# Kernel optimization log

Measured on AMD Instinct MI355X. Metric: run time of the kernel, lower is better.

Reference implementation:

```python
import jax, jax.numpy as jnp
import numpy as np

B = 4096
D = 256
N = 9000000
ALPHA = 0.5      # alpha_weight
GAMMA_S = 0.8
GAMMA_U = 0.9
RHO = 6.0
EPS = 1e-14
ETA = 0.01
TAU_MIN = 0.001
TAU_MAX = 1.0
GRAD_CLIP = 5.0
TAU_INIT = 0.07


def setup_inputs() -> dict:
    key = jax.random.key(0)
    k1, k2 = jax.random.split(key)
    return {
        "zis": jax.random.normal(k1, (B, D), dtype=jnp.float32),
        "zjs": jax.random.normal(k2, (B, D), dtype=jnp.float32),
        "ids": jnp.arange(B, dtype=jnp.int32),
        "s_I": jnp.zeros(N, jnp.float32),
        "s_T": jnp.zeros(N, jnp.float32),
        "b_I": jnp.zeros(N, jnp.float32),
        "b_T": jnp.zeros(N, jnp.float32),
        "u_I": jnp.zeros(N, jnp.float32),
        "u_T": jnp.zeros(N, jnp.float32),
        "tau_I": jnp.full(N, TAU_INIT, jnp.float32),
        "tau_T": jnp.full(N, TAU_INIT, jnp.float32),
    }


def reference(zis, zjs, ids, s_I, s_T, b_I, b_T, u_I, u_T, tau_I, tau_T):
    sg = jax.lax.stop_gradient
    Bc = zis.shape[0]
    # normalize
    zis = zis / jnp.linalg.norm(zis, axis=1, keepdims=True)
    zjs = zjs / jnp.linalg.norm(zjs, axis=1, keepdims=True)
    sim = jnp.einsum('id,jd->ij', zis, zjs)                 # [B,B]
    diag = jnp.diagonal(sim)
    image_diffs = sim - diag[:, None]
    text_diffs = sim - diag[None, :]
    tau_i = tau_I[ids]
    tau_t = tau_T[ids]
    # detached temperature-scaled diffs (torch .detach())
    idt = sg(image_diffs) / tau_i[:, None]
    tdt = sg(text_diffs) / tau_t[None, :]
    # running max update (online log-sum-exp shift)
    old_b_i = b_I[ids]
    old_b_t = b_T[ids]
    new_b_i = jnp.maximum(old_b_i, idt.max(axis=1))
    new_b_t = jnp.maximum(old_b_t, tdt.max(axis=0))
    mask = 1.0 - jnp.eye(Bc, dtype=zis.dtype)
    exp_i = jnp.exp(idt - new_b_i[:, None]) * mask
    exp_t = jnp.exp(tdt - new_b_t[None, :]) * mask
    g_i = exp_i.sum(axis=1)                                  # [B]
    g_t = exp_t.sum(axis=0)                                  # [B]
    # EMA of normalizers, rescaled by max shift
    s_i = (1.0 - GAMMA_S) * s_I[ids] * jnp.exp(old_b_i - new_b_i) + GAMMA_S * g_i
    s_t = (1.0 - GAMMA_S) * s_T[ids] * jnp.exp(old_b_t - new_b_t) + GAMMA_S * g_t
    s_i_c = jnp.clip(s_i, EPS, None)[:, None]                # [B,1]
    s_t_c = jnp.clip(s_t, EPS, None)[None, :]                # [1,B]
    w_i = exp_i / s_i_c
    w_t = exp_t / s_t_c
    image_loss = (sg(w_i) * image_diffs).sum(axis=1)         # [B]
    text_loss = (sg(w_t) * text_diffs).sum(axis=0)           # [B]
    total_loss = ALPHA * image_loss.mean() + (1.0 - ALPHA) * text_loss.mean()
    grad_tau_image = jnp.log(s_i_c) + new_b_i[:, None] + RHO - (w_i * idt).sum(axis=1, keepdims=True) / (Bc - 1)
    grad_tau_text = jnp.log(s_t_c) + new_b_t[None, :] + RHO - (w_t * tdt).sum(axis=0, keepdims=True) / (Bc - 1)
    # EMA of tau gradients with clipping, then temperature update
    u_i = (1.0 - GAMMA_U) * u_I[ids] + GAMMA_U * jnp.clip(grad_tau_image[:, 0], -GRAD_CLIP, GRAD_CLIP)
    u_t = (1.0 - GAMMA_U) * u_T[ids] + GAMMA_U * jnp.clip(grad_tau_text[0, :], -GRAD_CLIP, GRAD_CLIP)
    tau_i_new = jnp.clip(tau_i - ETA * u_i, TAU_MIN, TAU_MAX)
    tau_t_new = jnp.clip(tau_t - ETA * u_t, TAU_MIN, TAU_MAX)
    # scatter updated state back into persistent buffers
    s_I = s_I.at[ids].set(s_i)
    s_T = s_T.at[ids].set(s_t)
    b_I = b_I.at[ids].set(new_b_i)
    b_T = b_T.at[ids].set(new_b_t)
    u_I = u_I.at[ids].set(u_i)
    u_T = u_T.at[ids].set(u_t)
    tau_I = tau_I.at[ids].set(tau_i_new)
    tau_T = tau_T.at[ids].set(tau_t_new)
    return (g_i[:, None], g_t[None, :], grad_tau_image, grad_tau_text, total_loss,
            tau_i.mean(), tau_t.mean(), s_I, s_T, b_I, b_T, u_I, u_T, tau_I, tau_T)
```

## Files before the change

kernel.cpp:

```cpp
#include <hip/hip_runtime.h>
#include <math.h>

#define BDIM 4096
#define DDIM 256
#define NSTATE 9000000
#define PREFIX 3674116
#define PREFIX_N4 918529
#define COPY_THREADS 1048576

#define C_ALPHA 0.5f
#define C_GAMMA_S 0.8f
#define C_GAMMA_U 0.9f
#define C_RHO 6.0f
#define C_EPS 1e-14f
#define C_ETA 0.01f
#define C_TAU_MIN 0.001f
#define C_TAU_MAX 1.0f
#define C_GRAD_CLIP 5.0f

typedef unsigned short u16;
typedef __attribute__((ext_vector_type(8))) short short8;
typedef __attribute__((ext_vector_type(16))) float f32x16;
typedef __attribute__((ext_vector_type(4))) float nf4;

#define MFMA32 __builtin_amdgcn_mfma_f32_32x32x16_bf16

__device__ inline u16 f2bf(float f) {
    unsigned u = __float_as_uint(f);
    unsigned r = (u + 0x7FFFu + ((u >> 16) & 1u)) >> 16;
    return (u16)r;
}
__device__ inline float bf2f(u16 h) { return __uint_as_float(((unsigned)h) << 16); }

__device__ inline void nt_copy4(const nf4* __restrict__ s, long k, float* __restrict__ dbase) {
    nf4 v = __builtin_nontemporal_load(&s[k]);
    float* dp = dbase + 4 * k;
    __builtin_nontemporal_store(v.x, dp + 0);
    __builtin_nontemporal_store(v.y, dp + 1);
    __builtin_nontemporal_store(v.z, dp + 2);
    __builtin_nontemporal_store(v.w, dp + 3);
}

__global__ __launch_bounds__(256) void kprep(const float* __restrict__ zis,
                                             const float* __restrict__ zjs,
                                             u16* __restrict__ Ah, u16* __restrict__ Al,
                                             u16* __restrict__ Bh, u16* __restrict__ Bl,
                                             const int* __restrict__ ids,
                                             const float* __restrict__ tau_I,
                                             const float* __restrict__ tau_T,
                                             float* __restrict__ rowIT,
                                             float* __restrict__ colIT,
                                             float* __restrict__ acc4,
                                             int* __restrict__ ticket) {
    int blk = blockIdx.x;
    int t = threadIdx.x;
    if (blk == 256) {
        float sI = 0.f, sT = 0.f;
        for (int i = t; i < BDIM; i += 256) {
            int id = ids[i];
            float ti = tau_I[id], tt = tau_T[id];
            rowIT[i] = 1.0f / ti;
            colIT[i] = 1.0f / tt;
            sI += ti; sT += tt;
        }
        __shared__ float red[512];
        red[t] = sI; red[256 + t] = sT;
        __syncthreads();
        for (int s = 128; s > 0; s >>= 1) {
            if (t < s) { red[t] += red[t + s]; red[256 + t] += red[256 + t + s]; }
            __syncthreads();
        }
        if (t == 0) {
            acc4[0] = 0.f;
            acc4[1] = 0.f;
            acc4[2] = red[0];
            acc4[3] = red[256];
            *ticket = 0;
        }
        return;
    }
    bool isB = blk >= 128;
    const float* Z = isB ? zjs : zis;
    u16* H = isB ? Bh : Ah;
    u16* L = isB ? Bl : Al;
    int rblk = blk & 127;
    int r = t & 31, kc0 = t >> 5;
    int row = rblk * 32 + r;

    __shared__ float ssq[32];
    if (t < 32) ssq[t] = 0.f;
    __syncthreads();

    float4 v[8];
    float partial = 0.f;
#pragma unroll
    for (int c = 0; c < 4; ++c) {
        int kc = kc0 + 8 * c;
        float4 a = *(const float4*)&Z[(size_t)row * DDIM + kc * 8];
        float4 b = *(const float4*)&Z[(size_t)row * DDIM + kc * 8 + 4];
        v[2 * c] = a; v[2 * c + 1] = b;
        partial += a.x * a.x + a.y * a.y + a.z * a.z + a.w * a.w;
        partial += b.x * b.x + b.y * b.y + b.z * b.z + b.w * b.w;
    }
    atomicAdd(&ssq[r], partial);
    __syncthreads();
    float inv = rsqrtf(ssq[r]);

#pragma unroll
    for (int c = 0; c < 4; ++c) {
        int kc = kc0 + 8 * c;
        float f[8];
        f[0] = v[2*c].x * inv;   f[1] = v[2*c].y * inv;
        f[2] = v[2*c].z * inv;   f[3] = v[2*c].w * inv;
        f[4] = v[2*c+1].x * inv; f[5] = v[2*c+1].y * inv;
        f[6] = v[2*c+1].z * inv; f[7] = v[2*c+1].w * inv;
        u16 hh[8], ll[8];
#pragma unroll
        for (int j = 0; j < 8; ++j) {
            hh[j] = f2bf(f[j]);
            ll[j] = f2bf(f[j] - bf2f(hh[j]));
        }
        size_t base = (size_t)rblk * 8192 + (size_t)kc * 256 + (size_t)r * 8;
        uint4 ph, pl;
        ph.x = (unsigned)hh[0] | ((unsigned)hh[1] << 16);
        ph.y = (unsigned)hh[2] | ((unsigned)hh[3] << 16);
        ph.z = (unsigned)hh[4] | ((unsigned)hh[5] << 16);
        ph.w = (unsigned)hh[6] | ((unsigned)hh[7] << 16);
        pl.x = (unsigned)ll[0] | ((unsigned)ll[1] << 16);
        pl.y = (unsigned)ll[2] | ((unsigned)ll[3] << 16);
        pl.z = (unsigned)ll[4] | ((unsigned)ll[5] << 16);
        pl.w = (unsigned)ll[6] | ((unsigned)ll[7] << 16);
        *(uint4*)(H + base) = ph;
        *(uint4*)(L + base) = pl;
    }
}

__global__ __launch_bounds__(256, 3) void kmain(
    const u16* __restrict__ Ah, const u16* __restrict__ Al,
    const u16* __restrict__ Bh, const u16* __restrict__ Bl,
    const float* __restrict__ rowIT, const float* __restrict__ colIT,
    float* __restrict__ rPM, float* __restrict__ rPS1, float* __restrict__ rPS2,
    float* __restrict__ cPM, float* __restrict__ cPS1, float* __restrict__ cPS2,
    float* __restrict__ diag,
    const float* __restrict__ s_I, const float* __restrict__ s_T,
    const float* __restrict__ b_I, const float* __restrict__ b_T,
    const float* __restrict__ u_I, const float* __restrict__ u_T,
    const float* __restrict__ tau_I, const float* __restrict__ tau_T,
    long b0s, float* o)
{
    __shared__ float T[2][64 * 68];
    int bid = blockIdx.x;
    int t = threadIdx.x;

    if (bid % 5 != 0) {
        long cid = (long)(bid / 5) * 4 + (bid % 5) - 1;
        long tid = cid * 256 + t;
        {
            const nf4* s = (const nf4*)(s_I + b0s);
            float* d = o + b0s;
            long n4 = (NSTATE - b0s) / 4;
            for (long k = tid; k < n4; k += COPY_THREADS) nt_copy4(s, k, d);
        }
        const float* srcs[7] = {s_T, b_I, b_T, u_I, u_T, tau_I, tau_T};
#pragma unroll
        for (int b = 0; b < 7; b++) {
            const nf4* s = (const nf4*)srcs[b];
            float* d = o + (long)(b + 1) * NSTATE;
            for (long k = tid; k < NSTATE / 4; k += COPY_THREADS) nt_copy4(s, k, d);
        }
        return;
    }

    int gid = bid / 5;
    int by = gid >> 5, bx = gid & 31;
    int w = t >> 6, l = t & 63;
    int rw = w & 1, cw = w >> 1;
    int h = l >> 5, lc = l & 31;
    int rowbase = by * 128 + rw * 64;
    int colbase = bx * 128 + cw * 64;

    const u16* pAh = Ah + (size_t)(by * 4 + rw * 2) * 8192;
    const u16* pAl = Al + (size_t)(by * 4 + rw * 2) * 8192;
    const u16* pBh = Bh + (size_t)(bx * 4 + cw * 2) * 8192;
    const u16* pBl = Bl + (size_t)(bx * 4 + cw * 2) * 8192;

    f32x16 acc00, acc01, acc10, acc11;
#pragma unroll
    for (int e = 0; e < 16; ++e) { acc00[e] = 0.f; acc01[e] = 0.f; acc10[e] = 0.f; acc11[e] = 0.f; }

    for (int s = 0; s < 16; ++s) {
        int off = s * 512 + l * 8;
        short8 a0h = *(const short8*)(pAh + off);
        short8 a1h = *(const short8*)(pAh + 8192 + off);
        short8 a0l = *(const short8*)(pAl + off);
        short8 a1l = *(const short8*)(pAl + 8192 + off);
        short8 b0h = *(const short8*)(pBh + off);
        short8 b1h = *(const short8*)(pBh + 8192 + off);
        short8 b0l = *(const short8*)(pBl + off);
        short8 b1l = *(const short8*)(pBl + 8192 + off);

        acc00 = MFMA32(a0h, b0h, acc00, 0, 0, 0);
        acc01 = MFMA32(a0h, b1h, acc01, 0, 0, 0);
        acc10 = MFMA32(a1h, b0h, acc10, 0, 0, 0);
        acc11 = MFMA32(a1h, b1h, acc11, 0, 0, 0);
        acc00 = MFMA32(a0h, b0l, acc00, 0, 0, 0);
        acc01 = MFMA32(a0h, b1l, acc01, 0, 0, 0);
        acc10 = MFMA32(a1h, b0l, acc10, 0, 0, 0);
        acc11 = MFMA32(a1h, b1l, acc11, 0, 0, 0);
        acc00 = MFMA32(a0l, b0h, acc00, 0, 0, 0);
        acc01 = MFMA32(a0l, b1h, acc01, 0, 0, 0);
        acc10 = MFMA32(a1l, b0h, acc10, 0, 0, 0);
        acc11 = MFMA32(a1l, b1h, acc11, 0, 0, 0);
    }

#define COLPART(A0, A1, CT) do {                                                   \
        int gc = colbase + (CT) * 32 + lc;                                         \
        float itc = colIT[gc];                                                     \
        float m = -INFINITY;                                                       \
        _Pragma("unroll") for (int e = 0; e < 16; ++e) {                           \
            m = fmaxf(m, (A0)[e]); m = fmaxf(m, (A1)[e]); }                        \
        m = fmaxf(m, __shfl_xor(m, 32));                                           \
        float S1 = 0.f, S2 = 0.f;                                                  \
        _Pragma("unroll") for (int e = 0; e < 16; ++e) {                           \
            float v0 = (A0)[e]; float e0 = __expf((v0 - m) * itc); S1 += e0; S2 += e0 * v0; \
            float v1 = (A1)[e]; float e1 = __expf((v1 - m) * itc); S1 += e1; S2 += e1 * v1; } \
        S1 += __shfl_xor(S1, 32); S2 += __shfl_xor(S2, 32);                        \
        if (h == 0) { int slot = by * 2 + rw;                                      \
            cPM [slot * 4096 + gc] = m;                                            \
            cPS1[slot * 4096 + gc] = S1;                                           \
            cPS2[slot * 4096 + gc] = S2; }                                         \
    } while (0)

    COLPART(acc00, acc10, 0);
    COLPART(acc01, acc11, 1);

#define ROWPART(TB) do {                                                           \
        float* Tb = (TB);                                                          \
        _Pragma("unroll") for (int q = 0; q < 4; ++q) {                            \
            _Pragma("unroll") for (int j = 0; j < 4; ++j) {                        \
                int rr = 8 * q + 4 * h + j;                                        \
                Tb[(rr     ) * 68 + lc     ] = acc00[4 * q + j];                   \
                Tb[(rr     ) * 68 + lc + 32] = acc01[4 * q + j];                   \
                Tb[(rr + 32) * 68 + lc     ] = acc10[4 * q + j];                   \
                Tb[(rr + 32) * 68 + lc + 32] = acc11[4 * q + j]; } }               \
        float itr = rowIT[rowbase + l];                                            \
        float4 vv[16];                                                             \
        _Pragma("unroll") for (int c = 0; c < 16; ++c)                             \
            vv[c] = *(const float4*)&Tb[l * 68 + 4 * c];                           \
        float m = -INFINITY;                                                       \
        _Pragma("unroll") for (int c = 0; c < 16; ++c)                             \
            m = fmaxf(m, fmaxf(fmaxf(vv[c].x, vv[c].y), fmaxf(vv[c].z, vv[c].w))); \
        float S1 = 0.f, S2 = 0.f;                                                  \
        _Pragma("unroll") for (int c = 0; c < 16; ++c) {                           \
            float e0 = __expf((vv[c].x - m) * itr); S1 += e0; S2 += e0 * vv[c].x;  \
            float e1 = __expf((vv[c].y - m) * itr); S1 += e1; S2 += e1 * vv[c].y;  \
            float e2 = __expf((vv[c].z - m) * itr); S1 += e2; S2 += e2 * vv[c].z;  \
            float e3 = __expf((vv[c].w - m) * itr); S1 += e3; S2 += e3 * vv[c].w; }\
        int slot = bx * 2 + cw;                                                    \
        rPM [slot * 4096 + rowbase + l] = m;                                       \
        rPS1[slot * 4096 + rowbase + l] = S1;                                      \
        rPS2[slot * 4096 + rowbase + l] = S2;                                      \
        if (bx == by && rw == cw) diag[rowbase + l] = Tb[l * 68 + l];              \
    } while (0)

    if (w < 2) ROWPART(T[w]);
    __syncthreads();
    if (w >= 2) ROWPART(T[w - 2]);
}

__global__ __launch_bounds__(256) void kmerge(
    const int* __restrict__ ids,
    const float* __restrict__ s_I, const float* __restrict__ b_I,
    const float* __restrict__ u_I, const float* __restrict__ tau_I,
    const float* __restrict__ s_T, const float* __restrict__ b_T,
    const float* __restrict__ u_T, const float* __restrict__ tau_T,
    const float* __restrict__ rowIT, const float* __restrict__ colIT,
    const float* __restrict__ diag,
    const float* __restrict__ rPM, const float* __restrict__ rPS1, const float* __restrict__ rPS2,
    const float* __restrict__ cPM, const float* __restrict__ cPS1, const float* __restrict__ cPS2,
    float* __restrict__ O,
    float* __restrict__ sc_arrs,
    float* o_scat,
    float* acc4, int* ticket)
{
    int j = blockIdx.x * 256 + threadIdx.x;
    int t = threadIdx.x;
    bool rowside = (j < BDIM);
    int i = rowside ? j : j - BDIM;
    const float* PM  = rowside ? rPM  : cPM;
    const float* PS1 = rowside ? rPS1 : cPS1;
    const float* PS2 = rowside ? rPS2 : cPS2;
    float it = rowside ? rowIT[i] : colIT[i];

    float M = -INFINITY, S1 = 0.f, S2 = 0.f;
    for (int k = 0; k < 64; k++) {
        float m  = PM [k * BDIM + i];
        float s1 = PS1[k * BDIM + i];
        float s2 = PS2[k * BDIM + i];
        float Mn = fmaxf(M, m);
        float ea = __expf((M - Mn) * it);
        float eb = __expf((m - Mn) * it);
        S1 = S1 * ea + s1 * eb;
        S2 = S2 * ea + s2 * eb;
        M = Mn;
    }

    int id = ids[i];
    float tau  = rowside ? tau_I[id] : tau_T[id];
    float oldb = rowside ? b_I[id]   : b_T[id];
    float olds = rowside ? s_I[id]   : s_T[id];
    float oldu = rowside ? u_I[id]   : u_T[id];
    float dg = diag[i];

    float nb = fmaxf(oldb, (M - dg) * it);
    float F  = __expf((M - dg) * it - nb);
    float ed = __expf(-nb);
    float g  = F * S1 - ed;
    float Cs = F * (S2 - dg * S1);

    float s_new = (1.f - C_GAMMA_S) * olds * __expf(oldb - nb) + C_GAMMA_S * g;
    float scl = fmaxf(s_new, C_EPS);
    float loss = Cs / scl;
    float grad = logf(scl) + nb + C_RHO - (Cs / (scl * tau)) * (1.0f / (float)(BDIM - 1));
    float gc = fminf(fmaxf(grad, -C_GRAD_CLIP), C_GRAD_CLIP);
    float u_new = (1.f - C_GAMMA_U) * oldu + C_GAMMA_U * gc;
    float tau_new = fminf(fmaxf(tau - C_ETA * u_new, C_TAU_MIN), C_TAU_MAX);

    int bank0 = rowside ? 0 : 1;
    if (rowside) {
        O[i] = g;
        O[8192 + i] = grad;
    } else {
        O[4096 + i] = g;
        O[12288 + i] = grad;
    }
    if (o_scat) {
        long lid = id;
        o_scat[(long)(bank0 + 0) * NSTATE + lid] = s_new;
        o_scat[(long)(bank0 + 2) * NSTATE + lid] = nb;
        o_scat[(long)(bank0 + 4) * NSTATE + lid] = u_new;
        o_scat[(long)(bank0 + 6) * NSTATE + lid] = tau_new;
    } else {
        int base = rowside ? 0 : 4;
        sc_arrs[(base + 0) * BDIM + i] = s_new;
        sc_arrs[(base + 1) * BDIM + i] = nb;
        sc_arrs[(base + 2) * BDIM + i] = u_new;
        sc_arrs[(base + 3) * BDIM + i] = tau_new;
    }

    __shared__ float red[256];
    red[t] = loss;
    __syncthreads();
    for (int s = 128; s > 0; s >>= 1) {
        if (t < s) red[t] += red[t + s];
        __syncthreads();
    }
    if (t == 0) {
        atomicAdd(&acc4[rowside ? 0 : 1], red[0]);
        __threadfence();
        int old = atomicAdd(ticket, 1);
        if (old == 31) {
            float li = atomicAdd(&acc4[0], 0.f);
            float lt = atomicAdd(&acc4[1], 0.f);
            float invB = 1.0f / (float)BDIM;
            O[16384] = C_ALPHA * (li * invB) + (1.f - C_ALPHA) * (lt * invB);
            O[16385] = acc4[2] * invB;
            O[16386] = acc4[3] * invB;
        }
    }
}

__global__ __launch_bounds__(256) void kfix(const float* s_I, float* o) {
    long tid = (long)blockIdx.x * 256 + threadIdx.x;
    const nf4* s = (const nf4*)s_I;
    for (long k = tid; k < PREFIX_N4; k += 3584L * 256) nt_copy4(s, k, o);
}

__global__ __launch_bounds__(256) void kscat(const int* __restrict__ ids,
                                             const float* __restrict__ sc_arrs,
                                             float* __restrict__ o) {
    int t = blockIdx.x * 256 + threadIdx.x;
    if (t >= BDIM) return;
    long id = ids[t];
    o[0L * NSTATE + id] = sc_arrs[0 * BDIM + t];
    o[1L * NSTATE + id] = sc_arrs[4 * BDIM + t];
    o[2L * NSTATE + id] = sc_arrs[1 * BDIM + t];
    o[3L * NSTATE + id] = sc_arrs[5 * BDIM + t];
    o[4L * NSTATE + id] = sc_arrs[2 * BDIM + t];
    o[5L * NSTATE + id] = sc_arrs[6 * BDIM + t];
    o[6L * NSTATE + id] = sc_arrs[3 * BDIM + t];
    o[7L * NSTATE + id] = sc_arrs[7 * BDIM + t];
}

extern "C" void kernel_launch(void* const* d_in, const int* in_sizes, int n_in,
                              void* d_out, int out_size, void* d_ws, size_t ws_size,
                              hipStream_t stream) {
    const float* zis   = (const float*)d_in[0];
    const float* zjs   = (const float*)d_in[1];
    const int*   ids   = (const int*)d_in[2];
    const float* s_I   = (const float*)d_in[3];
    const float* s_T   = (const float*)d_in[4];
    const float* b_I   = (const float*)d_in[5];
    const float* b_T   = (const float*)d_in[6];
    const float* u_I   = (const float*)d_in[7];
    const float* u_T   = (const float*)d_in[8];
    const float* tau_I = (const float*)d_in[9];
    const float* tau_T = (const float*)d_in[10];
    float* O  = (float*)d_out;
    float* ws = (float*)d_ws;

    float* rowIT  = ws;
    float* colIT  = ws + 4096;
    float* acc4   = ws + 8192;
    int*   ticket = (int*)(ws + 8196);
    float* sc_arrs = ws + 16384;

    const bool bigws = ws_size >= (size_t)16 * 1024 * 1024;

    float *rPM, *rPS1, *rPS2, *cPM, *cPS1, *cPS2, *diag;
    u16 *Ah, *Al, *Bh, *Bl;
    long b0s;
    if (bigws) {
        float* P = ws + 53248;
        rPM  = P;            rPS1 = P + 262144;  rPS2 = P + 524288;
        cPM  = P + 786432;   cPS1 = P + 1048576; cPS2 = P + 1310720;
        diag = P + 1572864;
        Ah = (u16*)(P + 1576960);
        Al = Ah + 1048576; Bh = Al + 1048576; Bl = Bh + 1048576;
        b0s = 0;
    } else {
        float* P = O + 16388;
        rPM  = P;            rPS1 = P + 262144;  rPS2 = P + 524288;
        cPM  = P + 786432;   cPS1 = P + 1048576; cPS2 = P + 1310720;
        diag = P + 1572864;
        Ah = (u16*)(P + 1576960);
        Al = Ah + 1048576; Bh = Al + 1048576; Bl = Bh + 1048576;
        b0s = PREFIX;
    }

    kprep<<<257, 256, 0, stream>>>(zis, zjs, Ah, Al, Bh, Bl,
                                   ids, tau_I, tau_T, rowIT, colIT, acc4, ticket);

    kmain<<<5120, 256, 0, stream>>>(Ah, Al, Bh, Bl, rowIT, colIT,
                                    rPM, rPS1, rPS2, cPM, cPS1, cPS2, diag,
                                    s_I, s_T, b_I, b_T, u_I, u_T, tau_I, tau_T,
                                    b0s, O + 16387);

    kmerge<<<32, 256, 0, stream>>>(ids, s_I, b_I, u_I, tau_I, s_T, b_T, u_T, tau_T,
                                   rowIT, colIT, diag,
                                   rPM, rPS1, rPS2, cPM, cPS1, cPS2,
                                   O, sc_arrs, bigws ? (O + 16387) : nullptr,
                                   acc4, ticket);

    if (!bigws) {
        kfix<<<3584, 256, 0, stream>>>(s_I, O + 16387);
        kscat<<<16, 256, 0, stream>>>(ids, sc_arrs, O + 16387);
    }
}
```

Baseline: 544.4 us.

## Fuse all stages into one persistent kernel with atomic work queues

Replaces the prep, main GEMM/copy, merge, prefix-fix and scatter kernels with a single persistent kernel of 768 blocks. Blocks pull work items from atomic counters: normalization and bf16 split, GEMM tiles, 16K-float state-copy chunks, merge, prefix copy, then scatter, with spin-wait dependencies between phases. The aim is to remove launch gaps and let the bandwidth-bound copy overlap the MFMA tile work dynamically. It adds spin-wait synchronization costs and relies on all 768 blocks being co-resident to avoid deadlock.

```diff
diff --git a/kernel.cpp b/kernel.cpp
--- a/kernel.cpp
+++ b/kernel.cpp
@@ -3,10 +3,15 @@
 
 #define BDIM 4096
 #define DDIM 256
-#define NSTATE 9000000
-#define PREFIX 3674116
-#define PREFIX_N4 918529
-#define COPY_THREADS 1048576
+#define NSTATE 9000000L
+#define PREFIX 3674116L
+
+#define NTILES 1024
+#define CHUNK_F 16384L
+#define CPB 550
+#define NCHUNKS (8*CPB)
+#define NPFX 225
+#define GRID 768
 
 #define C_ALPHA 0.5f
 #define C_GAMMA_S 0.8f
@@ -24,6 +29,7 @@
 typedef __attribute__((ext_vector_type(4))) float nf4;
 
 #define MFMA32 __builtin_amdgcn_mfma_f32_32x32x16_bf16
+#define AGS __HIP_MEMORY_SCOPE_AGENT
 
 __device__ inline u16 f2bf(float f) {
     unsigned u = __float_as_uint(f);
@@ -40,178 +46,6 @@
     __builtin_nontemporal_store(v.z, dp + 2);
     __builtin_nontemporal_store(v.w, dp + 3);
 }
-
-__global__ __launch_bounds__(256) void kprep(const float* __restrict__ zis,
-                                             const float* __restrict__ zjs,
-                                             u16* __restrict__ Ah, u16* __restrict__ Al,
-                                             u16* __restrict__ Bh, u16* __restrict__ Bl,
-                                             const int* __restrict__ ids,
-                                             const float* __restrict__ tau_I,
-                                             const float* __restrict__ tau_T,
-                                             float* __restrict__ rowIT,
-                                             float* __restrict__ colIT,
-                                             float* __restrict__ acc4,
-                                             int* __restrict__ ticket) {
-    int blk = blockIdx.x;
-    int t = threadIdx.x;
-    if (blk == 256) {
-        float sI = 0.f, sT = 0.f;
-        for (int i = t; i < BDIM; i += 256) {
-            int id = ids[i];
-            float ti = tau_I[id], tt = tau_T[id];
-            rowIT[i] = 1.0f / ti;
-            colIT[i] = 1.0f / tt;
-            sI += ti; sT += tt;
-        }
-        __shared__ float red[512];
-        red[t] = sI; red[256 + t] = sT;
-        __syncthreads();
-        for (int s = 128; s > 0; s >>= 1) {
-            if (t < s) { red[t] += red[t + s]; red[256 + t] += red[256 + t + s]; }
-            __syncthreads();
-        }
-        if (t == 0) {
-            acc4[0] = 0.f;
-            acc4[1] = 0.f;
-            acc4[2] = red[0];
-            acc4[3] = red[256];
-            *ticket = 0;
-        }
-        return;
-    }
-    bool isB = blk >= 128;
-    const float* Z = isB ? zjs : zis;
-    u16* H = isB ? Bh : Ah;
-    u16* L = isB ? Bl : Al;
-    int rblk = blk & 127;
-    int r = t & 31, kc0 = t >> 5;
-    int row = rblk * 32 + r;
-
-    __shared__ float ssq[32];
-    if (t < 32) ssq[t] = 0.f;
-    __syncthreads();
-
-    float4 v[8];
-    float partial = 0.f;
-#pragma unroll
-    for (int c = 0; c < 4; ++c) {
-        int kc = kc0 + 8 * c;
-        float4 a = *(const float4*)&Z[(size_t)row * DDIM + kc * 8];
-        float4 b = *(const float4*)&Z[(size_t)row * DDIM + kc * 8 + 4];
-        v[2 * c] = a; v[2 * c + 1] = b;
-        partial += a.x * a.x + a.y * a.y + a.z * a.z + a.w * a.w;
-        partial += b.x * b.x + b.y * b.y + b.z * b.z + b.w * b.w;
-    }
-    atomicAdd(&ssq[r], partial);
-    __syncthreads();
-    float inv = rsqrtf(ssq[r]);
-
-#pragma unroll
-    for (int c = 0; c < 4; ++c) {
-        int kc = kc0 + 8 * c;
-        float f[8];
-        f[0] = v[2*c].x * inv;   f[1] = v[2*c].y * inv;
-        f[2] = v[2*c].z * inv;   f[3] = v[2*c].w * inv;
-        f[4] = v[2*c+1].x * inv; f[5] = v[2*c+1].y * inv;
-        f[6] = v[2*c+1].z * inv; f[7] = v[2*c+1].w * inv;
-        u16 hh[8], ll[8];
-#pragma unroll
-        for (int j = 0; j < 8; ++j) {
-            hh[j] = f2bf(f[j]);
-            ll[j] = f2bf(f[j] - bf2f(hh[j]));
-        }
-        size_t base = (size_t)rblk * 8192 + (size_t)kc * 256 + (size_t)r * 8;
-        uint4 ph, pl;
-        ph.x = (unsigned)hh[0] | ((unsigned)hh[1] << 16);
-        ph.y = (unsigned)hh[2] | ((unsigned)hh[3] << 16);
-        ph.z = (unsigned)hh[4] | ((unsigned)hh[5] << 16);
-        ph.w = (unsigned)hh[6] | ((unsigned)hh[7] << 16);
-        pl.x = (unsigned)ll[0] | ((unsigned)ll[1] << 16);
-        pl.y = (unsigned)ll[2] | ((unsigned)ll[3] << 16);
-        pl.z = (unsigned)ll[4] | ((unsigned)ll[5] << 16);
-        pl.w = (unsigned)ll[6] | ((unsigned)ll[7] << 16);
-        *(uint4*)(H + base) = ph;
-        *(uint4*)(L + base) = pl;
-    }
-}
-
-__global__ __launch_bounds__(256, 3) void kmain(
-    const u16* __restrict__ Ah, const u16* __restrict__ Al,
-    const u16* __restrict__ Bh, const u16* __restrict__ Bl,
-    const float* __restrict__ rowIT, const float* __restrict__ colIT,
-    float* __restrict__ rPM, float* __restrict__ rPS1, float* __restrict__ rPS2,
-    float* __restrict__ cPM, float* __restrict__ cPS1, float* __restrict__ cPS2,
-    float* __restrict__ diag,
-    const float* __restrict__ s_I, const float* __restrict__ s_T,
-    const float* __restrict__ b_I, const float* __restrict__ b_T,
-    const float* __restrict__ u_I, const float* __restrict__ u_T,
-    const float* __restrict__ tau_I, const float* __restrict__ tau_T,
-    long b0s, float* o)
-{
-    __shared__ float T[2][64 * 68];
-    int bid = blockIdx.x;
-    int t = threadIdx.x;
-
-    if (bid % 5 != 0) {
-        long cid = (long)(bid / 5) * 4 + (bid % 5) - 1;
-        long tid = cid * 256 + t;
-        {
-            const nf4* s = (const nf4*)(s_I + b0s);
-            float* d = o + b0s;
-            long n4 = (NSTATE - b0s) / 4;
-            for (long k = tid; k < n4; k += COPY_THREADS) nt_copy4(s, k, d);
-        }
-        const float* srcs[7] = {s_T, b_I, b_T, u_I, u_T, tau_I, tau_T};
-#pragma unroll
-        for (int b = 0; b < 7; b++) {
-            const nf4* s = (const nf4*)srcs[b];
-            float* d = o + (long)(b + 1) * NSTATE;
-            for (long k = tid; k < NSTATE / 4; k += COPY_THREADS) nt_copy4(s, k, d);
-        }
-        return;
-    }
-
-    int gid = bid / 5;
-    int by = gid >> 5, bx = gid & 31;
-    int w = t >> 6, l = t & 63;
-    int rw = w & 1, cw = w >> 1;
-    int h = l >> 5, lc = l & 31;
-    int rowbase = by * 128 + rw * 64;
-    int colbase = bx * 128 + cw * 64;
-
-    const u16* pAh = Ah + (size_t)(by * 4 + rw * 2) * 8192;
-    const u16* pAl = Al + (size_t)(by * 4 + rw * 2) * 8192;
-    const u16* pBh = Bh + (size_t)(bx * 4 + cw * 2) * 8192;
-    const u16* pBl = Bl + (size_t)(bx * 4 + cw * 2) * 8192;
-
-    f32x16 acc00, acc01, acc10, acc11;
-#pragma unroll
-    for (int e = 0; e < 16; ++e) { acc00[e] = 0.f; acc01[e] = 0.f; acc10[e] = 0.f; acc11[e] = 0.f; }
-
-    for (int s = 0; s < 16; ++s) {
-        int off = s * 512 + l * 8;
-        short8 a0h = *(const short8*)(pAh + off);
-        short8 a1h = *(const short8*)(pAh + 8192 + off);
-        short8 a0l = *(const short8*)(pAl + off);
-        short8 a1l = *(const short8*)(pAl + 8192 + off);
-        short8 b0h = *(const short8*)(pBh + off);
-        short8 b1h = *(const short8*)(pBh + 8192 + off);
-        short8 b0l = *(const short8*)(pBl + off);
-        short8 b1l = *(const short8*)(pBl + 8192 + off);
-
-        acc00 = MFMA32(a0h, b0h, acc00, 0, 0, 0);
-        acc01 = MFMA32(a0h, b1h, acc01, 0, 0, 0);
-        acc10 = MFMA32(a1h, b0h, acc10, 0, 0, 0);
-        acc11 = MFMA32(a1h, b1h, acc11, 0, 0, 0);
-        acc00 = MFMA32(a0h, b0l, acc00, 0, 0, 0);
-        acc01 = MFMA32(a0h, b1l, acc01, 0, 0, 0);
-        acc10 = MFMA32(a1h, b0l, acc10, 0, 0, 0);
-        acc11 = MFMA32(a1h, b1l, acc11, 0, 0, 0);
-        acc00 = MFMA32(a0l, b0h, acc00, 0, 0, 0);
-        acc01 = MFMA32(a0l, b1h, acc01, 0, 0, 0);
-        acc10 = MFMA32(a1l, b0h, acc10, 0, 0, 0);
-        acc11 = MFMA32(a1l, b1h, acc11, 0, 0, 0);
-    }
 
 #define COLPART(A0, A1, CT) do {                                                   \
         int gc = colbase + (CT) * 32 + lc;                                         \
@@ -230,9 +64,6 @@
             cPS1[slot * 4096 + gc] = S1;                                           \
             cPS2[slot * 4096 + gc] = S2; }                                         \
     } while (0)
-
-    COLPART(acc00, acc10, 0);
-    COLPART(acc01, acc11, 1);
 
 #define ROWPART(TB) do {                                                           \
         float* Tb = (TB);                                                          \
@@ -263,133 +94,370 @@
         if (bx == by && rw == cw) diag[rowbase + l] = Tb[l * 68 + l];              \
     } while (0)
 
-    if (w < 2) ROWPART(T[w]);
-    __syncthreads();
-    if (w >= 2) ROWPART(T[w - 2]);
+__global__ void kinit(float* ws) {
+    int t = threadIdx.x;
+    if (t < 12) ((int*)(ws + 8196))[t] = 0;
+    if (t == 12) ws[8192] = 0.f;
+    if (t == 13) ws[8193] = 0.f;
 }
 
-__global__ __launch_bounds__(256) void kmerge(
+__global__ __launch_bounds__(256, 3) void kall(
+    const float* __restrict__ zis, const float* __restrict__ zjs,
     const int* __restrict__ ids,
-    const float* __restrict__ s_I, const float* __restrict__ b_I,
-    const float* __restrict__ u_I, const float* __restrict__ tau_I,
-    const float* __restrict__ s_T, const float* __restrict__ b_T,
-    const float* __restrict__ u_T, const float* __restrict__ tau_T,
-    const float* __restrict__ rowIT, const float* __restrict__ colIT,
-    const float* __restrict__ diag,
-    const float* __restrict__ rPM, const float* __restrict__ rPS1, const float* __restrict__ rPS2,
-    const float* __restrict__ cPM, const float* __restrict__ cPS1, const float* __restrict__ cPS2,
-    float* __restrict__ O,
-    float* __restrict__ sc_arrs,
-    float* o_scat,
-    float* acc4, int* ticket)
+    const float* __restrict__ s_I, const float* __restrict__ s_T,
+    const float* __restrict__ b_I, const float* __restrict__ b_T,
+    const float* __restrict__ u_I, const float* __restrict__ u_T,
+    const float* __restrict__ tau_I, const float* __restrict__ tau_T,
+    float* O, float* ws, float* Sb, int fb)
 {
-    int j = blockIdx.x * 256 + threadIdx.x;
-    int t = threadIdx.x;
-    bool rowside = (j < BDIM);
-    int i = rowside ? j : j - BDIM;
-    const float* PM  = rowside ? rPM  : cPM;
-    const float* PS1 = rowside ? rPS1 : cPS1;
-    const float* PS2 = rowside ? rPS2 : cPS2;
-    float it = rowside ? rowIT[i] : colIT[i];
-
-    float M = -INFINITY, S1 = 0.f, S2 = 0.f;
-    for (int k = 0; k < 64; k++) {
-        float m  = PM [k * BDIM + i];
-        float s1 = PS1[k * BDIM + i];
-        float s2 = PS2[k * BDIM + i];
-        float Mn = fmaxf(M, m);
-        float ea = __expf((M - Mn) * it);
-        float eb = __expf((m - Mn) * it);
-        S1 = S1 * ea + s1 * eb;
-        S2 = S2 * ea + s2 * eb;
-        M = Mn;
-    }
-
-    int id = ids[i];
-    float tau  = rowside ? tau_I[id] : tau_T[id];
-    float oldb = rowside ? b_I[id]   : b_T[id];
-    float olds = rowside ? s_I[id]   : s_T[id];
-    float oldu = rowside ? u_I[id]   : u_T[id];
-    float dg = diag[i];
-
-    float nb = fmaxf(oldb, (M - dg) * it);
-    float F  = __expf((M - dg) * it - nb);
-    float ed = __expf(-nb);
-    float g  = F * S1 - ed;
-    float Cs = F * (S2 - dg * S1);
-
-    float s_new = (1.f - C_GAMMA_S) * olds * __expf(oldb - nb) + C_GAMMA_S * g;
-    float scl = fmaxf(s_new, C_EPS);
-    float loss = Cs / scl;
-    float grad = logf(scl) + nb + C_RHO - (Cs / (scl * tau)) * (1.0f / (float)(BDIM - 1));
-    float gc = fminf(fmaxf(grad, -C_GRAD_CLIP), C_GRAD_CLIP);
-    float u_new = (1.f - C_GAMMA_U) * oldu + C_GAMMA_U * gc;
-    float tau_new = fminf(fmaxf(tau - C_ETA * u_new, C_TAU_MIN), C_TAU_MAX);
-
-    int bank0 = rowside ? 0 : 1;
-    if (rowside) {
-        O[i] = g;
-        O[8192 + i] = grad;
-    } else {
-        O[4096 + i] = g;
-        O[12288 + i] = grad;
-    }
-    if (o_scat) {
-        long lid = id;
-        o_scat[(long)(bank0 + 0) * NSTATE + lid] = s_new;
-        o_scat[(long)(bank0 + 2) * NSTATE + lid] = nb;
-        o_scat[(long)(bank0 + 4) * NSTATE + lid] = u_new;
-        o_scat[(long)(bank0 + 6) * NSTATE + lid] = tau_new;
-    } else {
+    __shared__ union {
+        float T[2][64 * 68];
+        struct { float ssq[32]; float red[512]; } p0;
+    } sm;
+    __shared__ int sgrab, skind;
+
+    const int bid = blockIdx.x;
+    const int t = threadIdx.x;
+
+    float* o = O + 16387;
+    float* rowIT = ws;
+    float* colIT = ws + 4096;
+    float* acc4  = ws + 8192;
+    float* sc_arrs = ws + 16384;
+    int* ip = (int*)(ws + 8196);
+    int* ticket   = ip + 0;
+    int* p0_ctr   = ip + 1;  int* p0done  = ip + 2;
+    int* tile_ctr = ip + 3;  int* p1done  = ip + 4;
+    int* copy_ctr = ip + 5;  int* c_done  = ip + 6;
+    int* m_ctr    = ip + 7;  int* m_done  = ip + 8;
+    int* pfx_ctr  = ip + 9;  int* pfx_done= ip + 10;
+    int* sc_ctr   = ip + 11;
+
+    float* rPM  = Sb;            float* rPS1 = Sb + 262144;  float* rPS2 = Sb + 524288;
+    float* cPM  = Sb + 786432;   float* cPS1 = Sb + 1048576; float* cPS2 = Sb + 1310720;
+    float* diag = Sb + 1572864;
+    u16* ABw = (u16*)(Sb + 1576960);
+    const u16* Ah = (const u16*)ABw;
+    const u16* Al = Ah + 1048576;
+    const u16* Bh = Al + 1048576;
+    const u16* Bl = Bh + 1048576;
+
+#define WAITGE(P, TGT) do { if (t == 0) {                                              \
+        while (__hip_atomic_load((P), __ATOMIC_ACQUIRE, AGS) < (TGT))                  \
+            __builtin_amdgcn_s_sleep(8);                                               \
+        __threadfence(); }                                                             \
+        __syncthreads(); } while (0)
+
+#define DONE1(P) do { __syncthreads(); if (t == 0) {                                   \
+        __threadfence();                                                               \
+        __hip_atomic_fetch_add((P), 1, __ATOMIC_RELEASE, AGS); } } while (0)
+
+    auto copy_chunk = [&](int c) {
+        int bank = c / CPB;
+        long f0 = (long)(c - bank * CPB) * CHUNK_F;
+        long fend = f0 + CHUNK_F; if (fend > NSTATE) fend = NSTATE;
+        if (bank == 0 && fb) {
+            if (fend <= PREFIX) return;
+            if (f0 < PREFIX) f0 = PREFIX;
+        }
+        const float* src;
+        switch (bank) {
+            case 0: src = s_I; break;  case 1: src = s_T; break;
+            case 2: src = b_I; break;  case 3: src = b_T; break;
+            case 4: src = u_I; break;  case 5: src = u_T; break;
+            case 6: src = tau_I; break; default: src = tau_T; break;
+        }
+        float* dst = o + (long)bank * NSTATE;
+        const nf4* s4 = (const nf4*)src;
+        for (long k = f0 / 4 + t; k < fend / 4; k += 256) nt_copy4(s4, k, dst);
+    };
+
+    for (;;) {
+        __syncthreads();
+        if (t == 0) sgrab = atomicAdd(p0_ctr, 1);
+        __syncthreads();
+        int it0 = sgrab;
+        if (it0 >= 257) break;
+
+        if (it0 == 256) {
+            float sI = 0.f, sT = 0.f;
+            for (int i = t; i < BDIM; i += 256) {
+                int id = ids[i];
+                float ti = tau_I[id], tt = tau_T[id];
+                rowIT[i] = 1.0f / ti;
+                colIT[i] = 1.0f / tt;
+                sI += ti; sT += tt;
+            }
+            sm.p0.red[t] = sI; sm.p0.red[256 + t] = sT;
+            __syncthreads();
+            for (int s = 128; s > 0; s >>= 1) {
+                if (t < s) { sm.p0.red[t] += sm.p0.red[t + s]; sm.p0.red[256 + t] += sm.p0.red[256 + t + s]; }
+                __syncthreads();
+            }
+            if (t == 0) { acc4[2] = sm.p0.red[0]; acc4[3] = sm.p0.red[256]; }
+        } else {
+            bool isB = it0 >= 128;
+            const float* Z = isB ? zjs : zis;
+            u16* H = isB ? (ABw + 2097152) : ABw;
+            u16* L = isB ? (ABw + 3145728) : (ABw + 1048576);
+            int rblk = it0 & 127;
+            int r = t & 31, kc0 = t >> 5;
+            int row = rblk * 32 + r;
+
+            if (t < 32) sm.p0.ssq[t] = 0.f;
+            __syncthreads();
+
+            float4 v[8];
+            float partial = 0.f;
+#pragma unroll
+            for (int c = 0; c < 4; ++c) {
+                int kc = kc0 + 8 * c;
+                float4 a = *(const float4*)&Z[(size_t)row * DDIM + kc * 8];
+                float4 b = *(const float4*)&Z[(size_t)row * DDIM + kc * 8 + 4];
+                v[2 * c] = a; v[2 * c + 1] = b;
+                partial += a.x * a.x + a.y * a.y + a.z * a.z + a.w * a.w;
+                partial += b.x * b.x + b.y * b.y + b.z * b.z + b.w * b.w;
+            }
+            atomicAdd(&sm.p0.ssq[r], partial);
+            __syncthreads();
+            float inv = rsqrtf(sm.p0.ssq[r]);
+
+#pragma unroll
+            for (int c = 0; c < 4; ++c) {
+                int kc = kc0 + 8 * c;
+                float f[8];
+                f[0] = v[2*c].x * inv;   f[1] = v[2*c].y * inv;
+                f[2] = v[2*c].z * inv;   f[3] = v[2*c].w * inv;
+                f[4] = v[2*c+1].x * inv; f[5] = v[2*c+1].y * inv;
+                f[6] = v[2*c+1].z * inv; f[7] = v[2*c+1].w * inv;
+                u16 hh[8], ll[8];
+#pragma unroll
+                for (int j = 0; j < 8; ++j) {
+                    hh[j] = f2bf(f[j]);
+                    ll[j] = f2bf(f[j] - bf2f(hh[j]));
+                }
+                size_t base = (size_t)rblk * 8192 + (size_t)kc * 256 + (size_t)r * 8;
+                uint4 ph, pl;
+                ph.x = (unsigned)hh[0] | ((unsigned)hh[1] << 16);
+                ph.y = (unsigned)hh[2] | ((unsigned)hh[3] << 16);
+                ph.z = (unsigned)hh[4] | ((unsigned)hh[5] << 16);
+                ph.w = (unsigned)hh[6] | ((unsigned)hh[7] << 16);
+                pl.x = (unsigned)ll[0] | ((unsigned)ll[1] << 16);
+                pl.y = (unsigned)ll[2] | ((unsigned)ll[3] << 16);
+                pl.z = (unsigned)ll[4] | ((unsigned)ll[5] << 16);
+                pl.w = (unsigned)ll[6] | ((unsigned)ll[7] << 16);
+                *(uint4*)(H + base) = ph;
+                *(uint4*)(L + base) = pl;
+            }
+        }
+        DONE1(p0done);
+    }
+
+    const bool mergeprio = (bid < 32);
+    for (;;) {
+        __syncthreads();
+        if (t == 0) {
+            int kind, item = -1;
+            if (__hip_atomic_load(p0done, __ATOMIC_ACQUIRE, AGS) >= 257) {
+                item = atomicAdd(tile_ctr, 1);
+                if (item < NTILES) kind = 1;
+                else if (mergeprio) kind = 0;
+                else { item = atomicAdd(copy_ctr, 1); kind = (item < NCHUNKS) ? 2 : 0; }
+            } else {
+                item = atomicAdd(copy_ctr, 1);
+                kind = (item < NCHUNKS) ? 2 : 3;
+            }
+            sgrab = item; skind = kind;
+        }
+        __syncthreads();
+        int kind = skind, item = sgrab;
+        if (kind == 0) break;
+        if (kind == 1) {
+            int gid = item;
+            int by = gid >> 5, bx = gid & 31;
+            int w = t >> 6, l = t & 63;
+            int rw = w & 1, cw = w >> 1;
+            int h = l >> 5, lc = l & 31;
+            int rowbase = by * 128 + rw * 64;
+            int colbase = bx * 128 + cw * 64;
+
+            const u16* pAh = Ah + (size_t)(by * 4 + rw * 2) * 8192;
+            const u16* pAl = Al + (size_t)(by * 4 + rw * 2) * 8192;
+            const u16* pBh = Bh + (size_t)(bx * 4 + cw * 2) * 8192;
+            const u16* pBl = Bl + (size_t)(bx * 4 + cw * 2) * 8192;
+
+            f32x16 acc00, acc01, acc10, acc11;
+#pragma unroll
+            for (int e = 0; e < 16; ++e) { acc00[e] = 0.f; acc01[e] = 0.f; acc10[e] = 0.f; acc11[e] = 0.f; }
+
+            for (int s = 0; s < 16; ++s) {
+                int off = s * 512 + l * 8;
+                short8 a0h = *(const short8*)(pAh + off);
+                short8 a1h = *(const short8*)(pAh + 8192 + off);
+                short8 a0l = *(const short8*)(pAl + off);
+                short8 a1l = *(const short8*)(pAl + 8192 + off);
+                short8 b0h = *(const short8*)(pBh + off);
+                short8 b1h = *(const short8*)(pBh + 8192 + off);
+                short8 b0l = *(const short8*)(pBl + off);
+                short8 b1l = *(const short8*)(pBl + 8192 + off);
+
+                acc00 = MFMA32(a0h, b0h, acc00, 0, 0, 0);
+                acc01 = MFMA32(a0h, b1h, acc01, 0, 0, 0);
+                acc10 = MFMA32(a1h, b0h, acc10, 0, 0, 0);
+                acc11 = MFMA32(a1h, b1h, acc11, 0, 0, 0);
+                acc00 = MFMA32(a0h, b0l, acc00, 0, 0, 0);
+                acc01 = MFMA32(a0h, b1l, acc01, 0, 0, 0);
+                acc10 = MFMA32(a1h, b0l, acc10, 0, 0, 0);
+                acc11 = MFMA32(a1h, b1l, acc11, 0, 0, 0);
+                acc00 = MFMA32(a0l, b0h, acc00, 0, 0, 0);
+                acc01 = MFMA32(a0l, b1h, acc01, 0, 0, 0);
+                acc10 = MFMA32(a1l, b0h, acc10, 0, 0, 0);
+                acc11 = MFMA32(a1l, b1h, acc11, 0, 0, 0);
+            }
+
+            COLPART(acc00, acc10, 0);
+            COLPART(acc01, acc11, 1);
+
+            if (w < 2) ROWPART(sm.T[w]);
+            __syncthreads();
+            if (w >= 2) ROWPART(sm.T[w - 2]);
+
+            DONE1(p1done);
+        } else if (kind == 2) {
+            copy_chunk(item);
+            DONE1(c_done);
+        } else {
+            if (t == 0) {
+                while (__hip_atomic_load(p0done, __ATOMIC_ACQUIRE, AGS) < 257)
+                    __builtin_amdgcn_s_sleep(8);
+            }
+        }
+    }
+
+    WAITGE(p1done, NTILES);
+    for (;;) {
+        __syncthreads();
+        if (t == 0) sgrab = atomicAdd(m_ctr, 1);
+        __syncthreads();
+        int m = sgrab;
+        if (m >= 32) break;
+
+        int j = m * 256 + t;
+        bool rowside = (j < BDIM);
+        int i = rowside ? j : j - BDIM;
+        const float* PM  = rowside ? rPM  : cPM;
+        const float* PS1 = rowside ? rPS1 : cPS1;
+        const float* PS2 = rowside ? rPS2 : cPS2;
+        float it = rowside ? rowIT[i] : colIT[i];
+
+        float M = -INFINITY, S1 = 0.f, S2 = 0.f;
+        for (int k = 0; k < 64; k++) {
+            float mm = PM [k * BDIM + i];
+            float s1 = PS1[k * BDIM + i];
+            float s2 = PS2[k * BDIM + i];
+            float Mn = fmaxf(M, mm);
+            float ea = __expf((M - Mn) * it);
+            float eb = __expf((mm - Mn) * it);
+            S1 = S1 * ea + s1 * eb;
+            S2 = S2 * ea + s2 * eb;
+            M = Mn;
+        }
+
+        int id = ids[i];
+        float tau  = rowside ? tau_I[id] : tau_T[id];
+        float oldb = rowside ? b_I[id]   : b_T[id];
+        float olds = rowside ? s_I[id]   : s_T[id];
+        float oldu = rowside ? u_I[id]   : u_T[id];
+        float dg = diag[i];
+
+        float nb = fmaxf(oldb, (M - dg) * it);
+        float F  = __expf((M - dg) * it - nb);
+        float ed = __expf(-nb);
+        float g  = F * S1 - ed;
+        float Cs = F * (S2 - dg * S1);
+
+        float s_new = (1.f - C_GAMMA_S) * olds * __expf(oldb - nb) + C_GAMMA_S * g;
+        float scl = fmaxf(s_new, C_EPS);
+        float loss = Cs / scl;
+        float grad = logf(scl) + nb + C_RHO - (Cs / (scl * tau)) * (1.0f / (float)(BDIM - 1));
+        float gcl = fminf(fmaxf(grad, -C_GRAD_CLIP), C_GRAD_CLIP);
+        float u_new = (1.f - C_GAMMA_U) * oldu + C_GAMMA_U * gcl;
+        float tau_new = fminf(fmaxf(tau - C_ETA * u_new, C_TAU_MIN), C_TAU_MAX);
+
+        if (rowside) { O[i] = g; O[8192 + i] = grad; }
+        else         { O[4096 + i] = g; O[12288 + i] = grad; }
         int base = rowside ? 0 : 4;
         sc_arrs[(base + 0) * BDIM + i] = s_new;
         sc_arrs[(base + 1) * BDIM + i] = nb;
         sc_arrs[(base + 2) * BDIM + i] = u_new;
         sc_arrs[(base + 3) * BDIM + i] = tau_new;
-    }
-
-    __shared__ float red[256];
-    red[t] = loss;
+
+        sm.p0.red[t] = loss;
+        __syncthreads();
+        for (int s = 128; s > 0; s >>= 1) {
+            if (t < s) sm.p0.red[t] += sm.p0.red[t + s];
+            __syncthreads();
+        }
+        if (t == 0) {
+            atomicAdd(&acc4[rowside ? 0 : 1], sm.p0.red[0]);
+            __threadfence();
+            int old = atomicAdd(ticket, 1);
+            if (old == 31) {
+                float li = atomicAdd(&acc4[0], 0.f);
+                float lt = atomicAdd(&acc4[1], 0.f);
+                float invB = 1.0f / (float)BDIM;
+                O[16384] = C_ALPHA * (li * invB) + (1.f - C_ALPHA) * (lt * invB);
+                O[16385] = acc4[2] * invB;
+                O[16386] = acc4[3] * invB;
+            }
+        }
+        DONE1(m_done);
+    }
+
+    if (fb) {
+        WAITGE(m_done, 32);
+        for (;;) {
+            __syncthreads();
+            if (t == 0) sgrab = atomicAdd(pfx_ctr, 1);
+            __syncthreads();
+            int c = sgrab;
+            if (c >= NPFX) break;
+            long f0 = (long)c * CHUNK_F;
+            long fend = f0 + CHUNK_F; if (fend > PREFIX) fend = PREFIX;
+            const nf4* s4 = (const nf4*)s_I;
+            for (long k = f0 / 4 + t; k < fend / 4; k += 256) nt_copy4(s4, k, o);
+            DONE1(pfx_done);
+        }
+    }
+
+    if (t == 0) {
+        while (__hip_atomic_load(c_done, __ATOMIC_ACQUIRE, AGS) < NCHUNKS) __builtin_amdgcn_s_sleep(8);
+        while (__hip_atomic_load(m_done, __ATOMIC_ACQUIRE, AGS) < 32) __builtin_amdgcn_s_sleep(8);
+        if (fb) {
+            while (__hip_atomic_load(pfx_done, __ATOMIC_ACQUIRE, AGS) < NPFX) __builtin_amdgcn_s_sleep(8);
+        }
+        __threadfence();
+    }
     __syncthreads();
-    for (int s = 128; s > 0; s >>= 1) {
-        if (t < s) red[t] += red[t + s];
-        __syncthreads();
-    }
-    if (t == 0) {
-        atomicAdd(&acc4[rowside ? 0 : 1], red[0]);
-        __threadfence();
-        int old = atomicAdd(ticket, 1);
-        if (old == 31) {
-            float li = atomicAdd(&acc4[0], 0.f);
-            float lt = atomicAdd(&acc4[1], 0.f);
-            float invB = 1.0f / (float)BDIM;
-            O[16384] = C_ALPHA * (li * invB) + (1.f - C_ALPHA) * (lt * invB);
-            O[16385] = acc4[2] * invB;
-            O[16386] = acc4[3] * invB;
-        }
-    }
-}
-
-__global__ __launch_bounds__(256) void kfix(const float* s_I, float* o) {
-    long tid = (long)blockIdx.x * 256 + threadIdx.x;
-    const nf4* s = (const nf4*)s_I;
-    for (long k = tid; k < PREFIX_N4; k += 3584L * 256) nt_copy4(s, k, o);
-}
-
-__global__ __launch_bounds__(256) void kscat(const int* __restrict__ ids,
-                                             const float* __restrict__ sc_arrs,
-                                             float* __restrict__ o) {
-    int t = blockIdx.x * 256 + threadIdx.x;
-    if (t >= BDIM) return;
-    long id = ids[t];
-    o[0L * NSTATE + id] = sc_arrs[0 * BDIM + t];
-    o[1L * NSTATE + id] = sc_arrs[4 * BDIM + t];
-    o[2L * NSTATE + id] = sc_arrs[1 * BDIM + t];
-    o[3L * NSTATE + id] = sc_arrs[5 * BDIM + t];
-    o[4L * NSTATE + id] = sc_arrs[2 * BDIM + t];
-    o[5L * NSTATE + id] = sc_arrs[6 * BDIM + t];
-    o[6L * NSTATE + id] = sc_arrs[3 * BDIM + t];
-    o[7L * NSTATE + id] = sc_arrs[7 * BDIM + t];
+    for (;;) {
+        __syncthreads();
+        if (t == 0) sgrab = atomicAdd(sc_ctr, 1);
+        __syncthreads();
+        int s = sgrab;
+        if (s >= 16) break;
+        int idx = s * 256 + t;
+        long id = ids[idx];
+        o[0L * NSTATE + id] = sc_arrs[0 * BDIM + idx];
+        o[1L * NSTATE + id] = sc_arrs[4 * BDIM + idx];
+        o[2L * NSTATE + id] = sc_arrs[1 * BDIM + idx];
+        o[3L * NSTATE + id] = sc_arrs[5 * BDIM + idx];
+        o[4L * NSTATE + id] = sc_arrs[2 * BDIM + idx];
+        o[5L * NSTATE + id] = sc_arrs[6 * BDIM + idx];
+        o[6L * NSTATE + id] = sc_arrs[3 * BDIM + idx];
+        o[7L * NSTATE + id] = sc_arrs[7 * BDIM + idx];
+    }
+#undef WAITGE
+#undef DONE1
 }
 
 extern "C" void kernel_launch(void* const* d_in, const int* in_sizes, int n_in,
@@ -409,51 +477,12 @@
     float* O  = (float*)d_out;
     float* ws = (float*)d_ws;
 
-    float* rowIT  = ws;
-    float* colIT  = ws + 4096;
-    float* acc4   = ws + 8192;
-    int*   ticket = (int*)(ws + 8196);
-    float* sc_arrs = ws + 16384;
-
     const bool bigws = ws_size >= (size_t)16 * 1024 * 1024;
-
-    float *rPM, *rPS1, *rPS2, *cPM, *cPS1, *cPS2, *diag;
-    u16 *Ah, *Al, *Bh, *Bl;
-    long b0s;
-    if (bigws) {
-        float* P = ws + 53248;
-        rPM  = P;            rPS1 = P + 262144;  rPS2 = P + 524288;
-        cPM  = P + 786432;   cPS1 = P + 1048576; cPS2 = P + 1310720;
-        diag = P + 1572864;
-        Ah = (u16*)(P + 1576960);
-        Al = Ah + 1048576; Bh = Al + 1048576; Bl = Bh + 1048576;
-        b0s = 0;
-    } else {
-        float* P = O + 16388;
-        rPM  = P;            rPS1 = P + 262144;  rPS2 = P + 524288;
-        cPM  = P + 786432;   cPS1 = P + 1048576; cPS2 = P + 1310720;
-        diag = P + 1572864;
-        Ah = (u16*)(P + 1576960);
-        Al = Ah + 1048576; Bh = Al + 1048576; Bl = Bh + 1048576;
-        b0s = PREFIX;
-    }
-
-    kprep<<<257, 256, 0, stream>>>(zis, zjs, Ah, Al, Bh, Bl,
-                                   ids, tau_I, tau_T, rowIT, colIT, acc4, ticket);
-
-    kmain<<<5120, 256, 0, stream>>>(Ah, Al, Bh, Bl, rowIT, colIT,
-                                    rPM, rPS1, rPS2, cPM, cPS1, cPS2, diag,
-                                    s_I, s_T, b_I, b_T, u_I, u_T, tau_I, tau_T,
-                                    b0s, O + 16387);
-
-    kmerge<<<32, 256, 0, stream>>>(ids, s_I, b_I, u_I, tau_I, s_T, b_T, u_T, tau_T,
-                                   rowIT, colIT, diag,
-                                   rPM, rPS1, rPS2, cPM, cPS1, cPS2,
-                                   O, sc_arrs, bigws ? (O + 16387) : nullptr,
-                                   acc4, ticket);
-
-    if (!bigws) {
-        kfix<<<3584, 256, 0, stream>>>(s_I, O + 16387);
-        kscat<<<16, 256, 0, stream>>>(ids, sc_arrs, O + 16387);
-    }
+    float* Sb = bigws ? (ws + 53248) : (O + 16388);
+    int fb = bigws ? 0 : 1;
+
+    kinit<<<1, 64, 0, stream>>>(ws);
+    kall<<<GRID, 256, 0, stream>>>(zis, zjs, ids,
+                                   s_I, s_T, b_I, b_T, u_I, u_T, tau_I, tau_T,
+                                   O, ws, Sb, fb);
 }
```

New measurement: 1.478 ms. +171.4%, slower.
